# Optimization experiments

Measured on AMD Instinct MI355X. Metric: run time of the kernel, lower is better.

Reference implementation:

```python
import jax, jax.numpy as jnp
import numpy as np

B, T, D, H, W = 4, 16, 64, 64, 64
EXPAND = 4
D2 = 2 * D


def _ln(x, g, b, eps=1e-5):
    m = jnp.mean(x, axis=-1, keepdims=True)
    v = jnp.var(x, axis=-1, keepdims=True)
    return (x - m) * jax.lax.rsqrt(v + eps) * g + b


def _cnorm(z, g, b):
    # complex LayerNorm: LN over concatenated [real, imag] last dim
    zc = jnp.concatenate([z.real, z.imag], axis=-1)
    zn = _ln(zc, g, b)
    r, i = jnp.split(zn, 2, axis=-1)
    return r + 1j * i


def setup_inputs() -> dict:
    key = jax.random.key(0)
    ks = jax.random.split(key, 16)
    sD = 1.0 / np.sqrt(D)
    return {
        "x_real": jax.random.normal(ks[0], (B, T, D, H, W), jnp.float32),
        "x_imag": jax.random.normal(ks[1], (B, T, D, H, W), jnp.float32),
        "dt": jax.random.uniform(ks[2], (B,), jnp.float32, 0.5, 1.5),
        "ln_s_g": jnp.ones((D2,), jnp.float32),
        "ln_s_b": jnp.zeros((D2,), jnp.float32),
        "conv_w": jax.random.normal(ks[3], (D2, D2, 3, 3), jnp.float32) * 0.02,
        "conv_b": jnp.zeros((D2,), jnp.float32),
        "spec_wr": jax.random.normal(ks[4], (D, H, W), jnp.float32) * 0.1,
        "spec_wi": jax.random.normal(ks[5], (D, H, W), jnp.float32) * 0.1,
        "gate": jnp.full((1,), 0.5, jnp.float32),
        "ln_t_g": jnp.ones((D2,), jnp.float32),
        "ln_t_b": jnp.zeros((D2,), jnp.float32),
        "lam_r": -jnp.abs(jax.random.normal(ks[6], (D,), jnp.float32)) * 0.1 - 0.01,
        "lam_i": jax.random.normal(ks[7], (D,), jnp.float32) * 0.5,
        "enc_r": jax.random.normal(ks[8], (D, D), jnp.float32) * sD,
        "enc_i": jax.random.normal(ks[9], (D, D), jnp.float32) * sD,
        "dec_r": jax.random.normal(ks[10], (D, D), jnp.float32) * sD,
        "dec_i": jax.random.normal(ks[11], (D, D), jnp.float32) * sD,
        "p_w1": jax.random.normal(ks[12], (D2, D2 * EXPAND), jnp.float32) * 0.02,
        "p_b1": jnp.zeros((D2 * EXPAND,), jnp.float32),
        "p_w2": jax.random.normal(ks[13], (D2 * EXPAND, D2), jnp.float32) * 0.02,
        "p_b2": jnp.zeros((D2,), jnp.float32),
    }


def reference(x_real, x_imag, dt, ln_s_g, ln_s_b, conv_w, conv_b, spec_wr,
              spec_wi, gate, ln_t_g, ln_t_b, lam_r, lam_i, enc_r, enc_i,
              dec_r, dec_i, p_w1, p_b1, p_w2, p_b2):
    x = x_real + 1j * x_imag                                   # (B,T,D,H,W) c64
    # ---- spatial branch ----
    resid = x
    x_s = jnp.transpose(x.reshape(B * T, D, H, W), (0, 2, 3, 1))   # (BT,H,W,D)
    x_s = jnp.transpose(_cnorm(x_s, ln_s_g, ln_s_b), (0, 3, 1, 2)) # (BT,D,H,W)
    xri = jnp.concatenate([x_s.real, x_s.imag], axis=1)            # (BT,2D,H,W)
    oc = jax.lax.conv_general_dilated(
        xri, conv_w, (1, 1), 'SAME',
        dimension_numbers=('NCHW', 'OIHW', 'NCHW')) + conv_b[None, :, None, None]
    r, i = jnp.split(oc, 2, axis=1)
    cliff = r + 1j * i
    spec_w = spec_wr + 1j * spec_wi                                # (D,H,W)
    spec = jnp.fft.ifft2(jnp.fft.fft2(x_s, axes=(-2, -1)) * spec_w[None],
                         axes=(-2, -1))
    x_s = gate[0] * cliff + (1.0 - gate[0]) * spec
    x = x_s.reshape(B, T, D, H, W) + resid
    # ---- temporal branch: diagonal linear recurrence ----
    resid = x
    x_t = jnp.transpose(x, (0, 3, 4, 1, 2)).reshape(B, H * W, T, D)
    x_t = _cnorm(x_t, ln_t_g, ln_t_b)
    lam = lam_r + 1j * lam_i                                       # (D,)
    decay = jnp.exp(lam[None, :] * dt[:, None])                    # (B,D) c64
    forcing = (decay - 1.0) / lam[None, :]                         # ZOH input op
    E = enc_r + 1j * enc_i
    Dm = dec_r + 1j * dec_i
    x_eigen = jnp.einsum('bntd,de->bnte', x_t, E)                  # (B,HW,T,D)

    def step(h, u):                                                # h:(B,HW,D)
        h = h * decay[:, None, :] + u * forcing[:, None, :]
        return h, h

    h0 = jnp.zeros((B, H * W, D), jnp.complex64)
    _, h_eig = jax.lax.scan(step, h0, jnp.moveaxis(x_eigen, 2, 0))
    h_eig = jnp.moveaxis(h_eig, 0, 2)                              # (B,HW,T,D)
    dec = jnp.einsum('bntd,de->bnte', h_eig, Dm)
    x_drift = jnp.transpose(dec.real.reshape(B, H, W, T, D), (0, 3, 4, 1, 2))
    x = x_drift + resid
    # ---- para-pool channel MLP ----
    resid = x
    x_p = jnp.transpose(x, (0, 1, 3, 4, 2))                        # (B,T,H,W,D)
    xpf = jnp.concatenate([x_p.real, x_p.imag], axis=-1)           # (B,T,H,W,2D)
    h1 = jax.nn.gelu(jnp.einsum('bthwc,cf->bthwf', xpf, p_w1) + p_b1)
    h2 = jnp.einsum('bthwf,fc->bthwc', h1, p_w2) + p_b2
    r, i = jnp.split(h2, 2, axis=-1)
    x = jnp.transpose(r + 1j * i, (0, 1, 4, 2, 3)) + resid
    # return real representation: concat real/imag on channel axis
    return jnp.concatenate([x.real, x.imag], axis=2)               # (B,T,2D,H,W)
```

## Files before the change

### kernel.cpp

```cpp
#include <hip/hip_runtime.h>
#include <hip/hip_bf16.h>

#define NB 4
#define NT 16
#define ND 64
#define NHW 4096
#define NTOT (NB*NT*ND*NHW)

typedef __attribute__((ext_vector_type(8))) __bf16 bf16x8;
typedef __attribute__((ext_vector_type(4))) float f32x4;

__global__ void k_spec_reorder(const float* __restrict__ wr, const float* __restrict__ wi,
                               float* __restrict__ outr, float* __restrict__ outi) {
  int idx = blockIdx.x * 256 + threadIdx.x;
  int d = idx >> 12;
  int rc = idx & 4095;
  int r = rc >> 6, c = rc & 63;
  int br = __brev((unsigned)r) >> 26;
  int bc = __brev((unsigned)c) >> 26;
  int src = (d << 12) + (br << 6) + bc;
  outr[idx] = wr[src];
  outi[idx] = wi[src];
}

__global__ void k_ln(const float* __restrict__ xr, const float* __restrict__ xi,
                     const float* __restrict__ g, const float* __restrict__ b,
                     float* __restrict__ outr, float* __restrict__ outi) {
  int pos = blockIdx.x * 256 + threadIdx.x;
  int bt = pos >> 12;
  int hw = pos & 4095;
  size_t base = (size_t)bt * ND * NHW + hw;
  float s = 0.f, ss = 0.f;
  for (int d = 0; d < ND; ++d) {
    float r = xr[base + (size_t)d * NHW];
    float im = xi[base + (size_t)d * NHW];
    s += r + im; ss += r * r + im * im;
  }
  float mean = s * (1.0f / 128.0f);
  float var = ss * (1.0f / 128.0f) - mean * mean;
  float rstd = rsqrtf(var + 1e-5f);
  for (int d = 0; d < ND; ++d) {
    float r = xr[base + (size_t)d * NHW];
    float im = xi[base + (size_t)d * NHW];
    outr[base + (size_t)d * NHW] = (r - mean) * rstd * g[d] + b[d];
    outi[base + (size_t)d * NHW] = (im - mean) * rstd * g[64 + d] + b[64 + d];
  }
}

__global__ void k_wconv_repack(const float* __restrict__ w, __hip_bfloat16* __restrict__ wcp) {
  int idx = blockIdx.x * 256 + threadIdx.x;
  int j = idx & 7;
  int lane = (idx >> 3) & 63;
  int kt = (idx >> 9) & 3;
  int nt = (idx >> 11) & 7;
  int tap = idx >> 14;
  int ic = kt * 32 + (lane >> 4) * 8 + j;
  int oc = nt * 16 + (lane & 15);
  wcp[idx] = __float2bfloat16(w[((size_t)(oc * 128 + ic)) * 9 + tap]);
}

__global__ __launch_bounds__(256) void k_conv_mfma(
    const float* __restrict__ xsr, const float* __restrict__ xsi,
    const __hip_bfloat16* __restrict__ wcp, const float* __restrict__ bias,
    __hip_bfloat16* __restrict__ cr, __hip_bfloat16* __restrict__ ci) {
  __shared__ __align__(16) __bf16 lin[3 * 66 * 128];
  int blk = blockIdx.x;
  int y = blk & 63;
  int bt = blk >> 6;
  int tid = threadIdx.x;
  int lane = tid & 63, wave = tid >> 6;
  int lc = lane & 15, quad = lane >> 4;

  for (int i = tid; i < 48 * 66; i += 256) {
    int p = i / 66;
    int pos = i - p * 66;
    int ky = p >> 4, icg = p & 15;
    int gy = y + ky - 1, gx = pos - 1;
    float vals[8];
#pragma unroll
    for (int k = 0; k < 8; ++k) vals[k] = 0.f;
    if (gy >= 0 && gy < 64 && gx >= 0 && gx < 64) {
      const float* src = (icg < 8) ? xsr : xsi;
      size_t pbase = ((size_t)(bt * 64 + (icg & 7) * 8)) * NHW + gy * 64 + gx;
#pragma unroll
      for (int k = 0; k < 8; ++k) vals[k] = src[pbase + (size_t)k * NHW];
    }
    bf16x8 v;
#pragma unroll
    for (int k = 0; k < 8; ++k) v[k] = (__bf16)vals[k];
    int elem = ((ky * 66 + pos) * 128 + icg * 8) ^ ((pos & 7) << 3);
    *(bf16x8*)(lin + elem) = v;
  }
  __syncthreads();

  int mt0 = (wave >> 1) * 2;
  int ocb = (wave & 1) * 4;
  f32x4 acc[2][4];
#pragma unroll
  for (int m = 0; m < 2; ++m)
#pragma unroll
    for (int n = 0; n < 4; ++n) acc[m][n] = (f32x4){0.f, 0.f, 0.f, 0.f};

  for (int ky = 0; ky < 3; ++ky) {
#pragma unroll
    for (int kt = 0; kt < 4; ++kt) {
      bf16x8 a[3][2];
#pragma unroll
      for (int kx = 0; kx < 3; ++kx)
#pragma unroll
        for (int m = 0; m < 2; ++m) {
          int pos = (mt0 + m) * 16 + lc + kx;
          int elem = ((ky * 66 + pos) * 128 + kt * 32 + quad * 8) ^ ((pos & 7) << 3);
          a[kx][m] = *(const bf16x8*)(lin + elem);
        }
#pragma unroll
      for (int kx = 0; kx < 3; ++kx) {
        const __hip_bfloat16* wp =
            wcp + ((((size_t)(ky * 3 + kx) * 8 + ocb) * 4 + kt) * 64 + lane) * 8;
#pragma unroll
        for (int n = 0; n < 4; ++n) {
          bf16x8 b = *(const bf16x8*)(const void*)(wp + (size_t)n * (4 * 64 * 8));
#pragma unroll
          for (int m = 0; m < 2; ++m)
            acc[m][n] = __builtin_amdgcn_mfma_f32_16x16x32_bf16(a[kx][m], b, acc[m][n], 0, 0, 0);
        }
      }
    }
  }
  __syncthreads();

  __bf16* lout = lin;
#pragma unroll
  for (int n = 0; n < 4; ++n) {
    int oc = (ocb + n) * 16 + lc;
    float bb = bias[oc];
#pragma unroll
    for (int m = 0; m < 2; ++m)
#pragma unroll
      for (int r = 0; r < 4; ++r)
        lout[oc * 66 + (mt0 + m) * 16 + quad * 4 + r] = (__bf16)(acc[m][n][r] + bb);
  }
  __syncthreads();

  {
    int colh = (lane & 31) * 2;
    int ocl = lane >> 5;
#pragma unroll
    for (int it = 0; it < 16; ++it) {
      int oc = it * 8 + wave * 2 + ocl;
      __hip_bfloat16* dst = (oc < 64) ? cr : ci;
      size_t ob = ((size_t)(bt * 64 + (oc & 63))) * NHW + y * 64 + colh;
      *(unsigned int*)((void*)(dst + ob)) =
          *(const unsigned int*)((const void*)(lout + oc * 66 + colh));
    }
  }
}

__device__ __forceinline__ void fft64_fwd(float& re, float& im, int lane) {
#pragma unroll
  for (int m = 32; m >= 1; m >>= 1) {
    float pr = __shfl_xor(re, m, 64);
    float pi = __shfl_xor(im, m, 64);
    int j = lane & (m - 1);
    float ang = -3.14159265358979f * (float)j / (float)m;
    float s, c;
    __sincosf(ang, &s, &c);
    if (lane & m) {
      float tr = pr - re, ti = pi - im;
      re = tr * c - ti * s;
      im = tr * s + ti * c;
    } else { re += pr; im += pi; }
  }
}
__device__ __forceinline__ void fft64_inv(float& re, float& im, int lane) {
#pragma unroll
  for (int m = 1; m <= 32; m <<= 1) {
    int j = lane & (m - 1);
    float ang = 3.14159265358979f * (float)j / (float)m;
    float s, c;
    __sincosf(ang, &s, &c);
    float pr = __shfl_xor(re, m, 64);
    float pi = __shfl_xor(im, m, 64);
    if (lane & m) {
      float wr = re * c - im * s, wi = re * s + im * c;
      re = pr - wr; im = pi - wi;
    } else {
      float wr = pr * c - pi * s, wi = pr * s + pi * c;
      re += wr; im += wi;
    }
  }
}

__global__ __launch_bounds__(256) void k_fft_combine(
    float* xsr, float* xsi,
    const __hip_bfloat16* __restrict__ cr, const __hip_bfloat16* __restrict__ ci,
    const float* __restrict__ sbr, const float* __restrict__ sbi,
    const float* __restrict__ x0r, const float* __restrict__ x0i,
    const float* __restrict__ gate) {
  __shared__ float lr[64 * 65], li[64 * 65];
  int slice = blockIdx.x;
  int d = slice & 63;
  size_t base = (size_t)slice * NHW;
  int lane = threadIdx.x & 63, wv = threadIdx.x >> 6;
  float g = gate[0];
  for (int r = wv; r < 64; r += 4) {
    float re = xsr[base + r * 64 + lane];
    float im = xsi[base + r * 64 + lane];
    fft64_fwd(re, im, lane);
    lr[r * 65 + lane] = re; li[r * 65 + lane] = im;
  }
  __syncthreads();
  for (int c = wv; c < 64; c += 4) {
    float re = lr[lane * 65 + c], im = li[lane * 65 + c];
    fft64_fwd(re, im, lane);
    lr[lane * 65 + c] = re; li[lane * 65 + c] = im;
  }
  __syncthreads();
  for (int r = wv; r < 64; r += 4) {
    float re = lr[r * 65 + lane], im = li[r * 65 + lane];
    float sr = sbr[(size_t)d * NHW + r * 64 + lane];
    float si = sbi[(size_t)d * NHW + r * 64 + lane];
    float nr = re * sr - im * si, ni = re * si + im * sr;
    fft64_inv(nr, ni, lane);
    lr[r * 65 + lane] = nr * (1.0f / 64.0f);
    li[r * 65 + lane] = ni * (1.0f / 64.0f);
  }
  __syncthreads();
  for (int c = wv; c < 64; c += 4) {
    float re = lr[lane * 65 + c], im = li[lane * 65 + c];
    fft64_inv(re, im, lane);
    lr[lane * 65 + c] = re * (1.0f / 64.0f);
    li[lane * 65 + c] = im * (1.0f / 64.0f);
  }
  __syncthreads();
  for (int r = wv; r < 64; r += 4) {
    size_t off = base + r * 64 + lane;
    float spr = lr[r * 65 + lane], spi = li[r * 65 + lane];
    float outr = g * __bfloat162float(cr[off]) + (1.f - g) * spr + x0r[off];
    float outi = g * __bfloat162float(ci[off]) + (1.f - g) * spi + x0i[off];
    xsr[off] = outr; xsi[off] = outi;
  }
}

__global__ void k_repack_all(const float* __restrict__ w1, const float* __restrict__ w2,
                             const float* __restrict__ er, const float* __restrict__ ei,
                             const float* __restrict__ dmr, const float* __restrict__ dmi,
                             __hip_bfloat16* __restrict__ w1p, __hip_bfloat16* __restrict__ w2p,
                             __hip_bfloat16* __restrict__ encp, __hip_bfloat16* __restrict__ decp) {
  int idx = blockIdx.x * 256 + threadIdx.x;
  if (idx < 65536) {
    int j = idx & 7, lane = (idx >> 3) & 63, kt = (idx >> 9) & 3, nt = idx >> 11;
    int k = kt * 32 + (lane >> 4) * 8 + j;
    int n = nt * 16 + (lane & 15);
    w1p[idx] = __float2bfloat16(w1[k * 512 + n]);
  } else if (idx < 131072) {
    int i2 = idx - 65536;
    int j = i2 & 7, lane = (i2 >> 3) & 63, kt = (i2 >> 9) & 15, nt = i2 >> 13;
    int k = kt * 32 + (lane >> 4) * 8 + j;
    int n = nt * 16 + (lane & 15);
    w2p[i2] = __float2bfloat16(w2[k * 128 + n]);
  } else if (idx < 147456) {
    int i2 = idx - 131072;
    int j = i2 & 7, lane = (i2 >> 3) & 63, kt = (i2 >> 9) & 3, nt = i2 >> 11;
    int k = kt * 32 + (lane >> 4) * 8 + j;
    int n = nt * 16 + (lane & 15);
    float v;
    if (k < 64) v = (n < 64) ? er[k * 64 + n] : ei[k * 64 + (n - 64)];
    else        v = (n < 64) ? -ei[(k - 64) * 64 + n] : er[(k - 64) * 64 + (n - 64)];
    encp[i2] = __float2bfloat16(v);
  } else {
    int i2 = idx - 147456;
    int j = i2 & 7, lane = (i2 >> 3) & 63, kt = (i2 >> 9) & 3, nt = i2 >> 11;
    int k = kt * 32 + (lane >> 4) * 8 + j;
    int n = nt * 16 + (lane & 15);
    float v = (k < 64) ? dmr[k * 64 + n] : -dmi[(k - 64) * 64 + n];
    decp[i2] = __float2bfloat16(v);
  }
}

__global__ __launch_bounds__(256) void k_ln_enc(
    const float* __restrict__ xsr, const float* __restrict__ xsi,
    const float* __restrict__ lng, const float* __restrict__ lnb,
    const __hip_bfloat16* __restrict__ encp,
    __hip_bfloat16* __restrict__ xer, __hip_bfloat16* __restrict__ xei) {
  __shared__ __bf16 la[32 * 136];
  __shared__ float red_s[8][33], red_ss[8][33];
  int blk = blockIdx.x;
  int bt = blk >> 7;
  int hw0 = (blk & 127) << 5;
  int tid = threadIdx.x;
  int lane = tid & 63, wave = tid >> 6;
  int lc = lane & 15, quad = lane >> 4;
  int tok = tid & 31, cg = tid >> 5;
  float v[16];
  float s = 0.f, ss = 0.f;
#pragma unroll
  for (int it = 0; it < 16; ++it) {
    int c = it * 8 + cg;
    const float* src = (c < 64) ? (xsr + ((size_t)(bt * 64 + c)) * NHW)
                                : (xsi + ((size_t)(bt * 64 + c - 64)) * NHW);
    v[it] = src[hw0 + tok];
    s += v[it]; ss += v[it] * v[it];
  }
  red_s[cg][tok] = s; red_ss[cg][tok] = ss;
  __syncthreads();
  float S = 0.f, SS = 0.f;
#pragma unroll
  for (int k = 0; k < 8; ++k) { S += red_s[k][tok]; SS += red_ss[k][tok]; }
  float mean = S * (1.0f / 128.0f);
  float rstd = rsqrtf(SS * (1.0f / 128.0f) - mean * mean + 1e-5f);
#pragma unroll
  for (int it = 0; it < 16; ++it) {
    int c = it * 8 + cg;
    la[tok * 136 + c] = (__bf16)((v[it] - mean) * rstd * lng[c] + lnb[c]);
  }
  __syncthreads();
  f32x4 acc[2][2];
#pragma unroll
  for (int m = 0; m < 2; ++m)
#pragma unroll
    for (int n = 0; n < 2; ++n) acc[m][n] = (f32x4){0.f, 0.f, 0.f, 0.f};
#pragma unroll
  for (int kt = 0; kt < 4; ++kt) {
    bf16x8 a0 = *(const bf16x8*)&la[lc * 136 + kt * 32 + quad * 8];
    bf16x8 a1 = *(const bf16x8*)&la[(lc + 16) * 136 + kt * 32 + quad * 8];
#pragma unroll
    for (int n = 0; n < 2; ++n) {
      int ntg = wave * 2 + n;
      bf16x8 b = *(const bf16x8*)(const void*)(encp + (((size_t)ntg * 4 + kt) * 64 + lane) * 8);
      acc[0][n] = __builtin_amdgcn_mfma_f32_16x16x32_bf16(a0, b, acc[0][n], 0, 0, 0);
      acc[1][n] = __builtin_amdgcn_mfma_f32_16x16x32_bf16(a1, b, acc[1][n], 0, 0, 0);
    }
  }
  __syncthreads();
  __bf16* lo = la;
#pragma unroll
  for (int n = 0; n < 2; ++n) {
    int c = (wave * 2 + n) * 16 + lc;
#pragma unroll
    for (int m = 0; m < 2; ++m)
#pragma unroll
      for (int r = 0; r < 4; ++r)
        lo[c * 34 + m * 16 + quad * 4 + r] = (__bf16)acc[m][n][r];
  }
  __syncthreads();
  {
    int tokh = tid & 15, cc = tid >> 4;
#pragma unroll
    for (int it = 0; it < 8; ++it) {
      int c = it * 16 + cc;
      __hip_bfloat16* dst = (c < 64) ? xer : xei;
      size_t ob = ((size_t)(bt * 64 + (c & 63))) * NHW + hw0 + tokh * 2;
      *(unsigned int*)((void*)(dst + ob)) =
          *(const unsigned int*)((const void*)(lo + c * 34 + tokh * 2));
    }
  }
}

__global__ __launch_bounds__(256) void k_scan(
    __hip_bfloat16* xer, __hip_bfloat16* xei,
    const float* __restrict__ lam_r, const float* __restrict__ lam_i,
    const float* __restrict__ dtv) {
  int idx = blockIdx.x * 256 + threadIdx.x;
  int hw = idx & 4095;
  int e = (idx >> 12) & 63;
  int b = idx >> 18;
  float lrv = lam_r[e], liv = lam_i[e];
  float dtb = dtv[b];
  float mg = __expf(lrv * dtb);
  float sn, cs;
  __sincosf(liv * dtb, &sn, &cs);
  float der = mg * cs, dei = mg * sn;
  float nr = der - 1.0f, ni = dei;
  float dn = 1.0f / (lrv * lrv + liv * liv);
  float forr = (nr * lrv + ni * liv) * dn;
  float fori = (ni * lrv - nr * liv) * dn;
  float hr = 0.f, hi = 0.f;
  size_t base = ((size_t)(b * NT * ND + e)) * NHW + hw;
  for (int t = 0; t < NT; ++t) {
    size_t off = base + (size_t)t * ND * NHW;
    float ur = __bfloat162float(xer[off]);
    float ui = __bfloat162float(xei[off]);
    float h0r = hr, h0i = hi;
    hr = h0r * der - h0i * dei + ur * forr - ui * fori;
    hi = h0r * dei + h0i * der + ur * fori + ui * forr;
    xer[off] = __float2bfloat16(hr);
    xei[off] = __float2bfloat16(hi);
  }
}

__global__ __launch_bounds__(256) void k_dec(
    float* __restrict__ xsr,
    const __hip_bfloat16* __restrict__ her, const __hip_bfloat16* __restrict__ hei,
    const __hip_bfloat16* __restrict__ decp) {
  __shared__ __bf16 lh2[32 * 136];
  int blk = blockIdx.x;
  int bt = blk >> 7;
  int hw0 = (blk & 127) << 5;
  int tid = threadIdx.x;
  int lane = tid & 63, wave = tid >> 6;
  int lc = lane & 15, quad = lane >> 4;
  {
    int tok = tid & 31, cg = tid >> 5;
#pragma unroll
    for (int it = 0; it < 16; ++it) {
      int c = it * 8 + cg;
      const __hip_bfloat16* src = (c < 64) ? (her + ((size_t)(bt * 64 + c)) * NHW)
                                           : (hei + ((size_t)(bt * 64 + c - 64)) * NHW);
      lh2[tok * 136 + c] = ((const __bf16*)src)[hw0 + tok];
    }
  }
  __syncthreads();
  f32x4 acc[2];
  acc[0] = (f32x4){0.f, 0.f, 0.f, 0.f};
  acc[1] = (f32x4){0.f, 0.f, 0.f, 0.f};
#pragma unroll
  for (int kt = 0; kt < 4; ++kt) {
    bf16x8 a0 = *(const bf16x8*)&lh2[lc * 136 + kt * 32 + quad * 8];
    bf16x8 a1 = *(const bf16x8*)&lh2[(lc + 16) * 136 + kt * 32 + quad * 8];
    bf16x8 b = *(const bf16x8*)(const void*)(decp + (((size_t)wave * 4 + kt) * 64 + lane) * 8);
    acc[0] = __builtin_amdgcn_mfma_f32_16x16x32_bf16(a0, b, acc[0], 0, 0, 0);
    acc[1] = __builtin_amdgcn_mfma_f32_16x16x32_bf16(a1, b, acc[1], 0, 0, 0);
  }
  __syncthreads();
  float* lo = (float*)lh2;
  {
    int c = wave * 16 + lc;
#pragma unroll
    for (int m = 0; m < 2; ++m)
#pragma unroll
      for (int r = 0; r < 4; ++r)
        lo[c * 33 + m * 16 + quad * 4 + r] = acc[m][r];
  }
  __syncthreads();
  {
    int tok = tid & 31, cg = tid >> 5;
#pragma unroll
    for (int it = 0; it < 8; ++it) {
      int c = it * 8 + cg;
      size_t off = ((size_t)(bt * 64 + c)) * NHW + hw0 + tok;
      xsr[off] += lo[c * 33 + tok];
    }
  }
}

__global__ __launch_bounds__(256, 3) void k_mlp_mfma(
    const float* __restrict__ xsr, const float* __restrict__ xsi,
    const __hip_bfloat16* __restrict__ w1p, const __hip_bfloat16* __restrict__ w2p,
    const float* __restrict__ b1, const float* __restrict__ b2,
    float* __restrict__ out) {
  __shared__ __bf16 lf[32 * 136];
  __shared__ __bf16 lh[32 * 520];
  float* lo = (float*)lh;
  int blk = blockIdx.x;
  int bt = blk >> 7;
  int hw0 = (blk & 127) << 5;
  int tid = threadIdx.x;
  int lane = tid & 63, wave = tid >> 6;
  int lc = lane & 15, quad = lane >> 4;
  {
    int tok = tid & 31, cg = tid >> 5;
#pragma unroll
    for (int it = 0; it < 16; ++it) {
      int c = it * 8 + cg;
      const float* src = (c < 64) ? (xsr + ((size_t)(bt * 64 + c)) * NHW)
                                  : (xsi + ((size_t)(bt * 64 + c - 64)) * NHW);
      lf[tok * 136 + c] = (__bf16)src[hw0 + tok];
    }
  }
  __syncthreads();
  f32x4 acc[2][8];
#pragma unroll
  for (int mt = 0; mt < 2; ++mt)
#pragma unroll
    for (int nt = 0; nt < 8; ++nt) acc[mt][nt] = (f32x4){0.f, 0.f, 0.f, 0.f};
#pragma unroll
  for (int kt = 0; kt < 4; ++kt) {
    bf16x8 a0 = *(const bf16x8*)&lf[lc * 136 + kt * 32 + quad * 8];
    bf16x8 a1 = *(const bf16x8*)&lf[(lc + 16) * 136 + kt * 32 + quad * 8];
    const __hip_bfloat16* wp = w1p + (((size_t)(wave * 8) * 4 + kt) * 64 + lane) * 8;
#pragma unroll
    for (int nt = 0; nt < 8; ++nt) {
      bf16x8 b = *(const bf16x8*)(const void*)(wp + (size_t)nt * (4 * 64 * 8));
      acc[0][nt] = __builtin_amdgcn_mfma_f32_16x16x32_bf16(a0, b, acc[0][nt], 0, 0, 0);
      acc[1][nt] = __builtin_amdgcn_mfma_f32_16x16x32_bf16(a1, b, acc[1][nt], 0, 0, 0);
    }
  }
#pragma unroll
  for (int nt = 0; nt < 8; ++nt) {
    int col = wave * 128 + nt * 16 + lc;
    float bb = b1[col];
#pragma unroll
    for (int mt = 0; mt < 2; ++mt)
#pragma unroll
      for (int r = 0; r < 4; ++r) {
        float x = acc[mt][nt][r] + bb;
        float y = 0.7978845608f * (x + 0.044715f * x * x * x);
        float e = __expf(2.0f * y);
        float th = 1.0f - 2.0f / (e + 1.0f);
        float gv = 0.5f * x * (1.0f + th);
        lh[(mt * 16 + quad * 4 + r) * 520 + col] = (__bf16)gv;
      }
  }
  __syncthreads();
  f32x4 acc2[2][2];
#pragma unroll
  for (int mt = 0; mt < 2; ++mt)
#pragma unroll
    for (int n = 0; n < 2; ++n) acc2[mt][n] = (f32x4){0.f, 0.f, 0.f, 0.f};
#pragma unroll
  for (int kt = 0; kt < 16; ++kt) {
    bf16x8 a0 = *(const bf16x8*)&lh[lc * 520 + kt * 32 + quad * 8];
    bf16x8 a1 = *(const bf16x8*)&lh[(lc + 16) * 520 + kt * 32 + quad * 8];
#pragma unroll
    for (int n = 0; n < 2; ++n) {
      bf16x8 b = *(const bf16x8*)(const void*)(w2p + (((size_t)(wave * 2 + n) * 16 + kt) * 64 + lane) * 8);
      acc2[0][n] = __builtin_amdgcn_mfma_f32_16x16x32_bf16(a0, b, acc2[0][n], 0, 0, 0);
      acc2[1][n] = __builtin_amdgcn_mfma_f32_16x16x32_bf16(a1, b, acc2[1][n], 0, 0, 0);
    }
  }
  __syncthreads();
#pragma unroll
  for (int n = 0; n < 2; ++n) {
    int c = wave * 32 + n * 16 + lc;
    float bb = b2[c];
#pragma unroll
    for (int mt = 0; mt < 2; ++mt)
#pragma unroll
      for (int r = 0; r < 4; ++r)
        lo[c * 33 + mt * 16 + quad * 4 + r] = acc2[mt][n][r] + bb;
  }
  __syncthreads();
  {
    int tok = tid & 31, cg = tid >> 5;
#pragma unroll
    for (int it = 0; it < 16; ++it) {
      int c = it * 8 + cg;
      const float* src = (c < 64) ? (xsr + ((size_t)(bt * 64 + c)) * NHW)
                                  : (xsi + ((size_t)(bt * 64 + c - 64)) * NHW);
      out[((size_t)(bt * 128 + c)) * NHW + hw0 + tok] = lo[c * 33 + tok] + src[hw0 + tok];
    }
  }
}

extern "C" void kernel_launch(void* const* d_in, const int* in_sizes, int n_in,
                              void* d_out, int out_size, void* d_ws, size_t ws_size,
                              hipStream_t stream) {
  const float* x_r    = (const float*)d_in[0];
  const float* x_i    = (const float*)d_in[1];
  const float* dt     = (const float*)d_in[2];
  const float* ln_s_g = (const float*)d_in[3];
  const float* ln_s_b = (const float*)d_in[4];
  const float* conv_w = (const float*)d_in[5];
  const float* conv_b = (const float*)d_in[6];
  const float* spec_wr= (const float*)d_in[7];
  const float* spec_wi= (const float*)d_in[8];
  const float* gate   = (const float*)d_in[9];
  const float* ln_t_g = (const float*)d_in[10];
  const float* ln_t_b = (const float*)d_in[11];
  const float* lam_r  = (const float*)d_in[12];
  const float* lam_i  = (const float*)d_in[13];
  const float* enc_r  = (const float*)d_in[14];
  const float* enc_i  = (const float*)d_in[15];
  const float* dec_r  = (const float*)d_in[16];
  const float* dec_i  = (const float*)d_in[17];
  const float* p_w1   = (const float*)d_in[18];
  const float* p_b1   = (const float*)d_in[19];
  const float* p_w2   = (const float*)d_in[20];
  const float* p_b2   = (const float*)d_in[21];

  float* ws   = (float*)d_ws;
  float* xs_r = ws;
  float* xs_i = ws + (size_t)NTOT;
  float* sbr  = ws + (size_t)2 * NTOT;
  float* sbi  = sbr + (size_t)ND * NHW;
  __hip_bfloat16* cl_r = (__hip_bfloat16*)(sbi + (size_t)ND * NHW);
  __hip_bfloat16* cl_i = cl_r + (size_t)NTOT;
  __hip_bfloat16* sbpack = (__hip_bfloat16*)sbr;
  __hip_bfloat16* w1p  = sbpack;
  __hip_bfloat16* w2p  = sbpack + 65536;
  __hip_bfloat16* encp = sbpack + 131072;
  __hip_bfloat16* decp = sbpack + 147456;
  __hip_bfloat16* wcp = (__hip_bfloat16*)d_out;

  k_spec_reorder<<<1024, 256, 0, stream>>>(spec_wr, spec_wi, sbr, sbi);
  k_wconv_repack<<<576, 256, 0, stream>>>(conv_w, wcp);
  k_ln<<<1024, 256, 0, stream>>>(x_r, x_i, ln_s_g, ln_s_b, xs_r, xs_i);
  k_conv_mfma<<<4096, 256, 0, stream>>>(xs_r, xs_i, wcp, conv_b, cl_r, cl_i);
  k_fft_combine<<<4096, 256, 0, stream>>>(xs_r, xs_i, cl_r, cl_i, sbr, sbi, x_r, x_i, gate);
  k_repack_all<<<608, 256, 0, stream>>>(p_w1, p_w2, enc_r, enc_i, dec_r, dec_i,
                                        w1p, w2p, encp, decp);
  k_ln_enc<<<8192, 256, 0, stream>>>(xs_r, xs_i, ln_t_g, ln_t_b, encp, cl_r, cl_i);
  k_scan<<<4096, 256, 0, stream>>>(cl_r, cl_i, lam_r, lam_i, dt);
  k_dec<<<8192, 256, 0, stream>>>(xs_r, cl_r, cl_i, decp);
  k_mlp_mfma<<<8192, 256, 0, stream>>>(xs_r, xs_i, w1p, w2p, p_b1, p_b2, (float*)d_out);
}
```

Before: 940.8 us.

## Replace shuffle-based 2D FFT with bf16 MFMA DFT matrix multiplies

The radix-2 shuffle FFT over each 64x64 slice is replaced by four dense 64x128 DFT matrix multiplies using bf16 MFMA, with forward and inverse DFT matrices precomputed once in the repack kernel. The spectral weights are now read directly in natural order, so the bit-reversal reorder kernel is removed. This aims to move FFT arithmetic onto the matrix cores and cut shuffle and sincos work, at the cost of more FLOPs and bf16 rounding of the intermediates and DFT coefficients.

```diff
diff --git a/kernel.cpp b/kernel.cpp
--- a/kernel.cpp
+++ b/kernel.cpp
@@ -8,20 +8,8 @@
 #define NTOT (NB*NT*ND*NHW)
 
 typedef __attribute__((ext_vector_type(8))) __bf16 bf16x8;
+typedef __attribute__((ext_vector_type(4))) __bf16 bf16x4;
 typedef __attribute__((ext_vector_type(4))) float f32x4;
-
-__global__ void k_spec_reorder(const float* __restrict__ wr, const float* __restrict__ wi,
-                               float* __restrict__ outr, float* __restrict__ outi) {
-  int idx = blockIdx.x * 256 + threadIdx.x;
-  int d = idx >> 12;
-  int rc = idx & 4095;
-  int r = rc >> 6, c = rc & 63;
-  int br = __brev((unsigned)r) >> 26;
-  int bc = __brev((unsigned)c) >> 26;
-  int src = (d << 12) + (br << 6) + bc;
-  outr[idx] = wr[src];
-  outi[idx] = wi[src];
-}
 
 __global__ void k_ln(const float* __restrict__ xr, const float* __restrict__ xi,
                      const float* __restrict__ g, const float* __restrict__ b,
@@ -156,89 +144,124 @@
   }
 }
 
-__device__ __forceinline__ void fft64_fwd(float& re, float& im, int lane) {
-#pragma unroll
-  for (int m = 32; m >= 1; m >>= 1) {
-    float pr = __shfl_xor(re, m, 64);
-    float pi = __shfl_xor(im, m, 64);
-    int j = lane & (m - 1);
-    float ang = -3.14159265358979f * (float)j / (float)m;
-    float s, c;
-    __sincosf(ang, &s, &c);
-    if (lane & m) {
-      float tr = pr - re, ti = pi - im;
-      re = tr * c - ti * s;
-      im = tr * s + ti * c;
-    } else { re += pr; im += pi; }
-  }
-}
-__device__ __forceinline__ void fft64_inv(float& re, float& im, int lane) {
-#pragma unroll
-  for (int m = 1; m <= 32; m <<= 1) {
-    int j = lane & (m - 1);
-    float ang = 3.14159265358979f * (float)j / (float)m;
-    float s, c;
-    __sincosf(ang, &s, &c);
-    float pr = __shfl_xor(re, m, 64);
-    float pi = __shfl_xor(im, m, 64);
-    if (lane & m) {
-      float wr = re * c - im * s, wi = re * s + im * c;
-      re = pr - wr; im = pi - wi;
-    } else {
-      float wr = pr * c - pi * s, wi = pr * s + pi * c;
-      re += wr; im += wi;
-    }
-  }
-}
-
-__global__ __launch_bounds__(256) void k_fft_combine(
+__device__ __forceinline__ void gemm64x128(const __bf16* __restrict__ src,
+                                           const __hip_bfloat16* __restrict__ bp,
+                                           int lane, int lc, int quad, int w,
+                                           f32x4 (&acc)[4][2]) {
+#pragma unroll
+  for (int m = 0; m < 4; ++m)
+#pragma unroll
+    for (int n = 0; n < 2; ++n) acc[m][n] = (f32x4){0.f, 0.f, 0.f, 0.f};
+#pragma unroll
+  for (int kt = 0; kt < 4; ++kt) {
+    bf16x8 a[4];
+#pragma unroll
+    for (int m = 0; m < 4; ++m)
+      a[m] = *(const bf16x8*)&src[(m * 16 + lc) * 136 + kt * 32 + quad * 8];
+#pragma unroll
+    for (int n = 0; n < 2; ++n) {
+      int ntg = w + n * 4;
+      bf16x8 b = *(const bf16x8*)(const void*)(bp + (((size_t)ntg * 4 + kt) * 64 + lane) * 8);
+#pragma unroll
+      for (int m = 0; m < 4; ++m)
+        acc[m][n] = __builtin_amdgcn_mfma_f32_16x16x32_bf16(a[m], b, acc[m][n], 0, 0, 0);
+    }
+  }
+}
+__device__ __forceinline__ void store_T(__bf16* __restrict__ dst,
+                                        int lc, int quad, int w, f32x4 (&acc)[4][2]) {
+#pragma unroll
+  for (int m = 0; m < 4; ++m)
+#pragma unroll
+    for (int n = 0; n < 2; ++n) {
+      bf16x4 v;
+#pragma unroll
+      for (int r = 0; r < 4; ++r) v[r] = (__bf16)acc[m][n][r];
+      *(bf16x4*)&dst[(w * 16 + lc) * 136 + n * 64 + m * 16 + quad * 4] = v;
+    }
+}
+
+__global__ __launch_bounds__(256) void k_fft_mfma(
     float* xsr, float* xsi,
     const __hip_bfloat16* __restrict__ cr, const __hip_bfloat16* __restrict__ ci,
-    const float* __restrict__ sbr, const float* __restrict__ sbi,
+    const float* __restrict__ swr, const float* __restrict__ swi,
     const float* __restrict__ x0r, const float* __restrict__ x0i,
-    const float* __restrict__ gate) {
-  __shared__ float lr[64 * 65], li[64 * 65];
+    const float* __restrict__ gate,
+    const __hip_bfloat16* __restrict__ Fp, const __hip_bfloat16* __restrict__ Gp) {
+  __shared__ __align__(16) __bf16 lA[64 * 136];
+  __shared__ __align__(16) __bf16 lB[64 * 136];
   int slice = blockIdx.x;
   int d = slice & 63;
   size_t base = (size_t)slice * NHW;
-  int lane = threadIdx.x & 63, wv = threadIdx.x >> 6;
+  int tid = threadIdx.x, lane = tid & 63, w = tid >> 6;
+  int lc = lane & 15, quad = lane >> 4;
   float g = gate[0];
-  for (int r = wv; r < 64; r += 4) {
-    float re = xsr[base + r * 64 + lane];
-    float im = xsi[base + r * 64 + lane];
-    fft64_fwd(re, im, lane);
-    lr[r * 65 + lane] = re; li[r * 65 + lane] = im;
-  }
-  __syncthreads();
-  for (int c = wv; c < 64; c += 4) {
-    float re = lr[lane * 65 + c], im = li[lane * 65 + c];
-    fft64_fwd(re, im, lane);
-    lr[lane * 65 + c] = re; li[lane * 65 + c] = im;
-  }
-  __syncthreads();
-  for (int r = wv; r < 64; r += 4) {
-    float re = lr[r * 65 + lane], im = li[r * 65 + lane];
-    float sr = sbr[(size_t)d * NHW + r * 64 + lane];
-    float si = sbi[(size_t)d * NHW + r * 64 + lane];
-    float nr = re * sr - im * si, ni = re * si + im * sr;
-    fft64_inv(nr, ni, lane);
-    lr[r * 65 + lane] = nr * (1.0f / 64.0f);
-    li[r * 65 + lane] = ni * (1.0f / 64.0f);
-  }
-  __syncthreads();
-  for (int c = wv; c < 64; c += 4) {
-    float re = lr[lane * 65 + c], im = li[lane * 65 + c];
-    fft64_inv(re, im, lane);
-    lr[lane * 65 + c] = re * (1.0f / 64.0f);
-    li[lane * 65 + c] = im * (1.0f / 64.0f);
-  }
-  __syncthreads();
-  for (int r = wv; r < 64; r += 4) {
-    size_t off = base + r * 64 + lane;
-    float spr = lr[r * 65 + lane], spi = li[r * 65 + lane];
-    float outr = g * __bfloat162float(cr[off]) + (1.f - g) * spr + x0r[off];
-    float outi = g * __bfloat162float(ci[off]) + (1.f - g) * spi + x0i[off];
-    xsr[off] = outr; xsi[off] = outi;
+
+  {
+    int y = tid >> 2, xo = (tid & 3) * 4;
+#pragma unroll
+    for (int k = 0; k < 4; ++k) {
+      int x = xo + k * 16;
+      float4 vr = *(const float4*)(xsr + base + y * 64 + x);
+      float4 vi = *(const float4*)(xsi + base + y * 64 + x);
+      bf16x4 br_, bi_;
+#pragma unroll
+      for (int r = 0; r < 4; ++r) { br_[r] = (__bf16)(&vr.x)[r]; bi_[r] = (__bf16)(&vi.x)[r]; }
+      *(bf16x4*)&lA[y * 136 + x] = br_;
+      *(bf16x4*)&lA[y * 136 + 64 + x] = bi_;
+    }
+  }
+  __syncthreads();
+  f32x4 acc[4][2];
+  gemm64x128(lA, Fp, lane, lc, quad, w, acc);
+  store_T(lB, lc, quad, w, acc);
+  __syncthreads();
+  gemm64x128(lB, Fp, lane, lc, quad, w, acc);
+  {
+    int ky = w * 16 + lc;
+    const float* wrp = swr + (size_t)d * 4096 + ky * 64;
+    const float* wip = swi + (size_t)d * 4096 + ky * 64;
+#pragma unroll
+    for (int m = 0; m < 4; ++m) {
+      int kx0 = m * 16 + quad * 4;
+      float4 wr4 = *(const float4*)(wrp + kx0);
+      float4 wi4 = *(const float4*)(wip + kx0);
+      bf16x4 zr4, zi4;
+#pragma unroll
+      for (int r = 0; r < 4; ++r) {
+        float yr = acc[m][0][r], yi = acc[m][1][r];
+        float wr = (&wr4.x)[r], wi = (&wi4.x)[r];
+        zr4[r] = (__bf16)(yr * wr - yi * wi);
+        zi4[r] = (__bf16)(yr * wi + yi * wr);
+      }
+      *(bf16x4*)&lA[ky * 136 + kx0] = zr4;
+      *(bf16x4*)&lA[ky * 136 + 64 + kx0] = zi4;
+    }
+  }
+  __syncthreads();
+  gemm64x128(lA, Gp, lane, lc, quad, w, acc);
+  store_T(lB, lc, quad, w, acc);
+  __syncthreads();
+  gemm64x128(lB, Gp, lane, lc, quad, w, acc);
+  {
+    int y = w * 16 + lc;
+#pragma unroll
+    for (int m = 0; m < 4; ++m) {
+      int x = m * 16 + quad * 4;
+      size_t off = base + y * 64 + x;
+      float4 v0r = *(const float4*)(x0r + off);
+      float4 v0i = *(const float4*)(x0i + off);
+      bf16x4 c4r = *(const bf16x4*)((const __bf16*)cr + off);
+      bf16x4 c4i = *(const bf16x4*)((const __bf16*)ci + off);
+      float4 outr, outi;
+#pragma unroll
+      for (int r = 0; r < 4; ++r) {
+        (&outr.x)[r] = g * (float)c4r[r] + (1.f - g) * acc[m][0][r] + (&v0r.x)[r];
+        (&outi.x)[r] = g * (float)c4i[r] + (1.f - g) * acc[m][1][r] + (&v0i.x)[r];
+      }
+      *(float4*)(xsr + off) = outr;
+      *(float4*)(xsi + off) = outi;
+    }
   }
 }
 
@@ -246,7 +269,8 @@
                              const float* __restrict__ er, const float* __restrict__ ei,
                              const float* __restrict__ dmr, const float* __restrict__ dmi,
                              __hip_bfloat16* __restrict__ w1p, __hip_bfloat16* __restrict__ w2p,
-                             __hip_bfloat16* __restrict__ encp, __hip_bfloat16* __restrict__ decp) {
+                             __hip_bfloat16* __restrict__ encp, __hip_bfloat16* __restrict__ decp,
+                             __hip_bfloat16* __restrict__ fp, __hip_bfloat16* __restrict__ gp) {
   int idx = blockIdx.x * 256 + threadIdx.x;
   if (idx < 65536) {
     int j = idx & 7, lane = (idx >> 3) & 63, kt = (idx >> 9) & 3, nt = idx >> 11;
@@ -268,13 +292,33 @@
     if (k < 64) v = (n < 64) ? er[k * 64 + n] : ei[k * 64 + (n - 64)];
     else        v = (n < 64) ? -ei[(k - 64) * 64 + n] : er[(k - 64) * 64 + (n - 64)];
     encp[i2] = __float2bfloat16(v);
-  } else {
+  } else if (idx < 155648) {
     int i2 = idx - 147456;
     int j = i2 & 7, lane = (i2 >> 3) & 63, kt = (i2 >> 9) & 3, nt = i2 >> 11;
     int k = kt * 32 + (lane >> 4) * 8 + j;
     int n = nt * 16 + (lane & 15);
     float v = (k < 64) ? dmr[k * 64 + n] : -dmi[(k - 64) * 64 + n];
     decp[i2] = __float2bfloat16(v);
+  } else if (idx < 172032) {
+    int i2 = idx - 155648;
+    int j = i2 & 7, lane = (i2 >> 3) & 63, kt = (i2 >> 9) & 3, nt = i2 >> 11;
+    int k = kt * 32 + (lane >> 4) * 8 + j;
+    int n = nt * 16 + (lane & 15);
+    int p = ((k & 63) * (n & 63)) & 63;
+    float sv, cv;
+    __sincosf((float)p * 0.09817477042f, &sv, &cv);
+    float v = ((k < 64) == (n < 64)) ? cv : ((n >= 64) ? -sv : sv);
+    fp[i2] = __float2bfloat16(v);
+  } else {
+    int i2 = idx - 172032;
+    int j = i2 & 7, lane = (i2 >> 3) & 63, kt = (i2 >> 9) & 3, nt = i2 >> 11;
+    int k = kt * 32 + (lane >> 4) * 8 + j;
+    int n = nt * 16 + (lane & 15);
+    int p = ((k & 63) * (n & 63)) & 63;
+    float sv, cv;
+    __sincosf((float)p * 0.09817477042f, &sv, &cv);
+    float v = (((k < 64) == (n < 64)) ? cv : ((n >= 64) ? sv : -sv)) * 0.015625f;
+    gp[i2] = __float2bfloat16(v);
   }
 }
 
@@ -572,24 +616,24 @@
   float* ws   = (float*)d_ws;
   float* xs_r = ws;
   float* xs_i = ws + (size_t)NTOT;
-  float* sbr  = ws + (size_t)2 * NTOT;
-  float* sbi  = sbr + (size_t)ND * NHW;
-  __hip_bfloat16* cl_r = (__hip_bfloat16*)(sbi + (size_t)ND * NHW);
-  __hip_bfloat16* cl_i = cl_r + (size_t)NTOT;
-  __hip_bfloat16* sbpack = (__hip_bfloat16*)sbr;
+  __hip_bfloat16* sbpack = (__hip_bfloat16*)(ws + (size_t)2 * NTOT);
   __hip_bfloat16* w1p  = sbpack;
   __hip_bfloat16* w2p  = sbpack + 65536;
   __hip_bfloat16* encp = sbpack + 131072;
   __hip_bfloat16* decp = sbpack + 147456;
+  __hip_bfloat16* Fp   = sbpack + 155648;
+  __hip_bfloat16* Gp   = sbpack + 172032;
+  __hip_bfloat16* cl_r = (__hip_bfloat16*)(ws + (size_t)2 * NTOT + (size_t)2 * ND * NHW);
+  __hip_bfloat16* cl_i = cl_r + (size_t)NTOT;
   __hip_bfloat16* wcp = (__hip_bfloat16*)d_out;
 
-  k_spec_reorder<<<1024, 256, 0, stream>>>(spec_wr, spec_wi, sbr, sbi);
+  k_repack_all<<<736, 256, 0, stream>>>(p_w1, p_w2, enc_r, enc_i, dec_r, dec_i,
+                                        w1p, w2p, encp, decp, Fp, Gp);
   k_wconv_repack<<<576, 256, 0, stream>>>(conv_w, wcp);
   k_ln<<<1024, 256, 0, stream>>>(x_r, x_i, ln_s_g, ln_s_b, xs_r, xs_i);
   k_conv_mfma<<<4096, 256, 0, stream>>>(xs_r, xs_i, wcp, conv_b, cl_r, cl_i);
-  k_fft_combine<<<4096, 256, 0, stream>>>(xs_r, xs_i, cl_r, cl_i, sbr, sbi, x_r, x_i, gate);
-  k_repack_all<<<608, 256, 0, stream>>>(p_w1, p_w2, enc_r, enc_i, dec_r, dec_i,
-                                        w1p, w2p, encp, decp);
+  k_fft_mfma<<<4096, 256, 0, stream>>>(xs_r, xs_i, cl_r, cl_i, spec_wr, spec_wi,
+                                       x_r, x_i, gate, Fp, Gp);
   k_ln_enc<<<8192, 256, 0, stream>>>(xs_r, xs_i, ln_t_g, ln_t_b, encp, cl_r, cl_i);
   k_scan<<<4096, 256, 0, stream>>>(cl_r, cl_i, lam_r, lam_i, dt);
   k_dec<<<8192, 256, 0, stream>>>(xs_r, cl_r, cl_i, decp);
```

Measured after the change: 814.5 us. -13.4%, faster.
